# Kernel optimization log

Measured on AMD Instinct MI355X. Metric: run time of the kernel, lower is better.

The kernel has to match this reference:

```python
import jax, jax.numpy as jnp
import numpy as np

THRESHOLD = 0.5
EPS = 1e-6


def setup_inputs() -> dict:
    key = jax.random.key(0)
    k1, k2, k3 = jax.random.split(key, 3)
    B, C, T = 32, 6, 64
    K, N = 8, 128
    S, P = 32, 64
    points = jax.random.normal(k1, (B, C, T, 2), dtype=jnp.float32)
    road_boundary = jax.random.normal(k2, (B, K, N, 2), dtype=jnp.float32)
    centerlines = jax.random.normal(k3, (B, S, P, 2), dtype=jnp.float32)
    return {"points": points, "road_boundary": road_boundary, "centerlines": centerlines}


def _cross(v1, v2):
    return v1[..., 0] * v2[..., 1] - v1[..., 1] * v2[..., 0]


def reference(points, road_boundary, centerlines):
    B, C, T, _ = points.shape
    _, K, N, _ = road_boundary.shape
    _, S, P, _ = centerlines.shape

    # --- min distance to boundary segments ---
    seg_a = road_boundary[:, :, :-1, :]          # (B,K,N-1,2)
    seg_d = road_boundary[:, :, 1:, :] - seg_a   # (B,K,N-1,2)

    p = points[:, None, :, :, None, :]           # (B,1,C,T,1,2)
    a = seg_a[:, :, None, None, :, :]            # (B,K,1,1,N-1,2)
    d = seg_d[:, :, None, None, :, :]            # (B,K,1,1,N-1,2)

    v1 = p - a                                   # (B,K,C,T,N-1,2)
    dot = (v1 * d).sum(-1)                       # (B,K,C,T,N-1)
    edge_sq = (d * d).sum(-1)                    # (B,K,1,1,N-1)
    proj = jnp.clip(dot / (edge_sq + EPS), 0.0, 1.0)
    closest = a + d * proj[..., None]            # (B,K,C,T,N-1,2)
    dist = jnp.sqrt(((p - closest) ** 2).sum(-1))  # (B,K,C,T,N-1)
    min_dist = dist.min(axis=-1).min(axis=1)     # (B,C,T)

    # --- nearest centerline point ---
    cl = centerlines.reshape(B, S * P, 2)        # (B,SP,2)
    v2 = points[:, None, :, :, :] - cl[:, :, None, None, :]  # (B,SP,C,T,2)
    cl_dist_sq = (v2 ** 2).sum(-1)               # (B,SP,C,T)
    idx = jnp.argmin(cl_dist_sq, axis=1)         # (B,C,T)
    closest_cl = cl[jnp.arange(B)[:, None, None], idx]  # (B,C,T,2)

    # --- segment intersection test: (point -> nearest centerline pt) vs boundary edges ---
    a1 = points[:, None, None, :, :, :]          # (B,1,1,C,T,2)
    a2 = closest_cl[:, None, None, :, :, :]      # (B,1,1,C,T,2)
    b1 = seg_a[:, :, :, None, None, :]           # (B,K,N-1,1,1,2)
    db = seg_d[:, :, :, None, None, :]           # (B,K,N-1,1,1,2)

    da = a2 - a1
    dp = a1 - b1                                 # (B,K,N-1,C,T,2)
    dadb = _cross(da, db)                        # (B,K,N-1,C,T)
    t = _cross(da, dp) / (dadb + EPS)
    u = _cross(db, dp) / (dadb + EPS)
    intersect = (t >= 0.0) & (t <= 1.0) & (u >= 0.0) & (u <= 1.0)

    inside = ~jnp.any(intersect, axis=(1, 2))    # (B,C,T)
    min_dist = jnp.where(inside, -min_dist, min_dist)
    return jax.nn.relu(min_dist + THRESHOLD).sum(-1)  # (B,C)
```

## Files before the change

### kernel.cpp

```cpp
#include <hip/hip_runtime.h>

constexpr int cB = 32, cC = 6, cT = 64;
constexpr int cK = 8, cN = 128;
constexpr int cS = 32, cP = 64;
constexpr int NSEG_PAD = cK * cN;
constexpr int NCL  = cS * cP;
constexpr int G = 4;
constexpr int PPW = 4;
constexpr int NIT = NSEG_PAD / 64;
constexpr float F_EPS = 1e-6f;
constexpr float F_THRESHOLD = 0.5f;

__global__ __launch_bounds__(256) void offroad_kernel(
    const float* __restrict__ points,
    const float* __restrict__ road_boundary,
    const float* __restrict__ centerlines,
    float* __restrict__ out)
{
    const int blk  = blockIdx.x;
    const int g    = blk & (G - 1);
    const int bc   = blk >> 2;
    const int b    = bc / cC;
    const int lane = threadIdx.x & 63;
    const int wave = threadIdx.x >> 6;

    const float2* __restrict__ rb2 =
        (const float2*)(road_boundary + (size_t)b * cK * cN * 2);
    const float4* __restrict__ cl4 =
        (const float4*)(centerlines + (size_t)b * NCL * 2);

    const int t0 = (g << 4) | (wave << 2);
    const float* pb = points + (((size_t)bc) * cT + t0) * 2;
    float px[PPW], py[PPW];
    #pragma unroll
    for (int p = 0; p < PPW; ++p) { px[p] = pb[2 * p]; py[p] = pb[2 * p + 1]; }

    float min_d2[PPW], best_d2[PPW];
    int   best_i[PPW];
    #pragma unroll
    for (int p = 0; p < PPW; ++p) {
        min_d2[p] = 3.4e38f; best_d2[p] = 3.4e38f; best_i[p] = 0x7fffffff;
    }

    int s = lane;
    float2 a  = rb2[s];
    float2 nx = rb2[s + (((s & (cN - 1)) < cN - 1) ? 1 : 0)];
    float4 cp = cl4[s];

    #pragma unroll 4
    for (int i = 0; i < NIT; ++i) {
        const float2 ac = a;  const float2 nxc = nx;  const float4 cpc = cp;
        const int    sc = s;
        s += 64;
        if (i < NIT - 1) {
            a  = rb2[s];
            nx = rb2[s + (((s & (cN - 1)) < cN - 1) ? 1 : 0)];
            cp = cl4[s];
        }

        const float dx = nxc.x - ac.x, dy = nxc.y - ac.y;
        const float inv_e2 = __builtin_amdgcn_rcpf(dx * dx + dy * dy + F_EPS);
        const int ia = 2 * sc;

        #pragma unroll
        for (int p = 0; p < PPW; ++p) {
            float v1x = px[p] - ac.x, v1y = py[p] - ac.y;
            float proj = (v1x * dx + v1y * dy) * inv_e2;
            proj = fminf(fmaxf(proj, 0.0f), 1.0f);
            float ex = v1x - dx * proj;
            float ey = v1y - dy * proj;
            min_d2[p] = fminf(min_d2[p], ex * ex + ey * ey);

            float dxa = px[p] - cpc.x, dya = py[p] - cpc.y;
            float d2a = dxa * dxa + dya * dya;
            float dxb = px[p] - cpc.z, dyb = py[p] - cpc.w;
            float d2b = dxb * dxb + dyb * dyb;
            float dmin = d2a; int imin = ia;
            if (d2b < d2a) { dmin = d2b; imin = ia + 1; }
            if (dmin < best_d2[p] ||
                (dmin == best_d2[p] && imin < best_i[p])) {
                best_d2[p] = dmin; best_i[p] = imin;
            }
        }
    }

    #pragma unroll
    for (int off = 1; off <= 32; off <<= 1) {
        #pragma unroll
        for (int p = 0; p < PPW; ++p) {
            float od2 = __shfl_xor(best_d2[p], off);
            int   oi  = __shfl_xor(best_i[p], off);
            if (od2 < best_d2[p] || (od2 == best_d2[p] && oi < best_i[p])) {
                best_d2[p] = od2; best_i[p] = oi;
            }
        }
    }

    const float2* __restrict__ cl2 = (const float2*)cl4;
    float dax[PPW], day[PPW];
    #pragma unroll
    for (int p = 0; p < PPW; ++p) {
        float2 cc = cl2[best_i[p]];
        dax[p] = cc.x - px[p]; day[p] = cc.y - py[p];
    }

    int hit[PPW] = {0, 0, 0, 0};
    s = lane;
    a  = rb2[s];
    nx = rb2[s + (((s & (cN - 1)) < cN - 1) ? 1 : 0)];

    #pragma unroll 4
    for (int i = 0; i < NIT; ++i) {
        const float2 ac = a;  const float2 nxc = nx;
        const int    sc = s;
        s += 64;
        if (i < NIT - 1) {
            a  = rb2[s];
            nx = rb2[s + (((s & (cN - 1)) < cN - 1) ? 1 : 0)];
        }

        const float dbx = nxc.x - ac.x, dby = nxc.y - ac.y;
        const int valid = ((sc & (cN - 1)) < cN - 1) ? 1 : 0;

        #pragma unroll
        for (int p = 0; p < PPW; ++p) {
            float dpx = px[p] - ac.x, dpy = py[p] - ac.y;
            float w  = dax[p] * dby - day[p] * dbx + F_EPS;
            float w2 = w * w;
            float ct = (dax[p] * dpy - day[p] * dpx) * w;
            float cu = (dbx * dpy - dby * dpx) * w;
            bool inb = (ct >= 0.0f) & (ct <= w2) & (cu >= 0.0f) & (cu <= w2);
            hit[p] |= valid & (int)inb;
        }
    }

    #pragma unroll
    for (int off = 1; off <= 32; off <<= 1) {
        #pragma unroll
        for (int p = 0; p < PPW; ++p) {
            min_d2[p] = fminf(min_d2[p], __shfl_xor(min_d2[p], off));
            hit[p]   |= __shfl_xor(hit[p], off);
        }
    }

    float total = 0.0f;
    #pragma unroll
    for (int p = 0; p < PPW; ++p) {
        float md = sqrtf(min_d2[p]);
        float sd = hit[p] ? md : -md;
        total += fmaxf(sd + F_THRESHOLD, 0.0f);
    }
    if (lane == 0)
        atomicAdd(&out[bc], total);
}

extern "C" void kernel_launch(void* const* d_in, const int* in_sizes, int n_in,
                              void* d_out, int out_size, void* d_ws, size_t ws_size,
                              hipStream_t stream) {
    const float* points      = (const float*)d_in[0];
    const float* boundary    = (const float*)d_in[1];
    const float* centerlines = (const float*)d_in[2];
    float* out = (float*)d_out;
    hipMemsetAsync(out, 0, (size_t)out_size * sizeof(float), stream);
    offroad_kernel<<<cB * cC * G, 256, 0, stream>>>(points, boundary, centerlines, out);
}
```

Before: 83.78 us.

## Fuse boundary distance into intersection pass and share segment endpoints via shuffles

Moves the min-distance-to-boundary computation out of the centerline argmin loop and into the intersection loop, so both boundary computations reuse the same segment vectors and v1 differences. Each segment's next endpoint now comes from a wavefront shuffle (shfl_down plus a broadcast of the next chunk's first point) instead of a second global load. The projection clamp uses fmed3. The intersection loop gets heavier per iteration, and shuffle latency is added in exchange for fewer memory loads and redundant arithmetic.

```diff
diff --git a/kernel.cpp b/kernel.cpp
--- a/kernel.cpp
+++ b/kernel.cpp
@@ -35,55 +35,36 @@
     #pragma unroll
     for (int p = 0; p < PPW; ++p) { px[p] = pb[2 * p]; py[p] = pb[2 * p + 1]; }
 
-    float min_d2[PPW], best_d2[PPW];
+    float best_d2[PPW];
     int   best_i[PPW];
     #pragma unroll
-    for (int p = 0; p < PPW; ++p) {
-        min_d2[p] = 3.4e38f; best_d2[p] = 3.4e38f; best_i[p] = 0x7fffffff;
-    }
+    for (int p = 0; p < PPW; ++p) { best_d2[p] = 3.4e38f; best_i[p] = 0x7fffffff; }
 
-    int s = lane;
-    float2 a  = rb2[s];
-    float2 nx = rb2[s + (((s & (cN - 1)) < cN - 1) ? 1 : 0)];
-    float4 cp = cl4[s];
-
-    #pragma unroll 4
-    for (int i = 0; i < NIT; ++i) {
-        const float2 ac = a;  const float2 nxc = nx;  const float4 cpc = cp;
-        const int    sc = s;
-        s += 64;
-        if (i < NIT - 1) {
-            a  = rb2[s];
-            nx = rb2[s + (((s & (cN - 1)) < cN - 1) ? 1 : 0)];
-            cp = cl4[s];
-        }
-
-        const float dx = nxc.x - ac.x, dy = nxc.y - ac.y;
-        const float inv_e2 = __builtin_amdgcn_rcpf(dx * dx + dy * dy + F_EPS);
-        const int ia = 2 * sc;
-
-        #pragma unroll
-        for (int p = 0; p < PPW; ++p) {
-            float v1x = px[p] - ac.x, v1y = py[p] - ac.y;
-            float proj = (v1x * dx + v1y * dy) * inv_e2;
-            proj = fminf(fmaxf(proj, 0.0f), 1.0f);
-            float ex = v1x - dx * proj;
-            float ey = v1y - dy * proj;
-            min_d2[p] = fminf(min_d2[p], ex * ex + ey * ey);
-
-            float dxa = px[p] - cpc.x, dya = py[p] - cpc.y;
-            float d2a = dxa * dxa + dya * dya;
-            float dxb = px[p] - cpc.z, dyb = py[p] - cpc.w;
-            float d2b = dxb * dxb + dyb * dyb;
-            float dmin = d2a; int imin = ia;
-            if (d2b < d2a) { dmin = d2b; imin = ia + 1; }
-            if (dmin < best_d2[p] ||
-                (dmin == best_d2[p] && imin < best_i[p])) {
-                best_d2[p] = dmin; best_i[p] = imin;
+    {
+        int s = lane;
+        float4 cp = cl4[s];
+        #pragma unroll 4
+        for (int i = 0; i < NIT; ++i) {
+            const float4 cpc = cp;
+            const int sc = s;
+            s += 64;
+            if (i < NIT - 1) cp = cl4[s];
+            const int ia = 2 * sc;
+            #pragma unroll
+            for (int p = 0; p < PPW; ++p) {
+                float dxa = px[p] - cpc.x, dya = py[p] - cpc.y;
+                float d2a = dxa * dxa + dya * dya;
+                float dxb = px[p] - cpc.z, dyb = py[p] - cpc.w;
+                float d2b = dxb * dxb + dyb * dyb;
+                float dmin = d2a; int imin = ia;
+                if (d2b < d2a) { dmin = d2b; imin = ia + 1; }
+                if (dmin < best_d2[p] ||
+                    (dmin == best_d2[p] && imin < best_i[p])) {
+                    best_d2[p] = dmin; best_i[p] = imin;
+                }
             }
         }
     }
-
     #pragma unroll
     for (int off = 1; off <= 32; off <<= 1) {
         #pragma unroll
@@ -95,7 +76,6 @@
             }
         }
     }
-
     const float2* __restrict__ cl2 = (const float2*)cl4;
     float dax[PPW], day[PPW];
     #pragma unroll
@@ -104,33 +84,52 @@
         dax[p] = cc.x - px[p]; day[p] = cc.y - py[p];
     }
 
-    int hit[PPW] = {0, 0, 0, 0};
-    s = lane;
-    a  = rb2[s];
-    nx = rb2[s + (((s & (cN - 1)) < cN - 1) ? 1 : 0)];
+    float min_d2[PPW];
+    int   hit[PPW];
+    #pragma unroll
+    for (int p = 0; p < PPW; ++p) { min_d2[p] = 3.4e38f; hit[p] = 0; }
 
-    #pragma unroll 4
-    for (int i = 0; i < NIT; ++i) {
-        const float2 ac = a;  const float2 nxc = nx;
-        const int    sc = s;
-        s += 64;
-        if (i < NIT - 1) {
-            a  = rb2[s];
-            nx = rb2[s + (((s & (cN - 1)) < cN - 1) ? 1 : 0)];
-        }
+    {
+        int s = lane;
+        float2 a = rb2[s];
+        #pragma unroll 2
+        for (int i = 0; i < NIT; ++i) {
+            const float2 ac = a;
+            s += 64;
+            float2 an = ac;
+            if (i < NIT - 1) an = rb2[s];
 
-        const float dbx = nxc.x - ac.x, dby = nxc.y - ac.y;
-        const int valid = ((sc & (cN - 1)) < cN - 1) ? 1 : 0;
+            float sd_x = __shfl_down(ac.x, 1);
+            float sd_y = __shfl_down(ac.y, 1);
+            float b0x  = __shfl(an.x, 0);
+            float b0y  = __shfl(an.y, 0);
+            const bool last = (lane == 63);
+            const bool odd  = (i & 1) != 0;
+            float nx_x = last ? (odd ? ac.x : b0x) : sd_x;
+            float nx_y = last ? (odd ? ac.y : b0y) : sd_y;
+            const int valid = (last && odd) ? 0 : 1;
 
-        #pragma unroll
-        for (int p = 0; p < PPW; ++p) {
-            float dpx = px[p] - ac.x, dpy = py[p] - ac.y;
-            float w  = dax[p] * dby - day[p] * dbx + F_EPS;
-            float w2 = w * w;
-            float ct = (dax[p] * dpy - day[p] * dpx) * w;
-            float cu = (dbx * dpy - dby * dpx) * w;
-            bool inb = (ct >= 0.0f) & (ct <= w2) & (cu >= 0.0f) & (cu <= w2);
-            hit[p] |= valid & (int)inb;
+            a = an;
+
+            const float dx = nx_x - ac.x, dy = nx_y - ac.y;
+            const float inv_e2 =
+                __builtin_amdgcn_rcpf(dx * dx + dy * dy + F_EPS);
+
+            #pragma unroll
+            for (int p = 0; p < PPW; ++p) {
+                float v1x = px[p] - ac.x, v1y = py[p] - ac.y;
+                float proj = (v1x * dx + v1y * dy) * inv_e2;
+                proj = __builtin_amdgcn_fmed3f(proj, 0.0f, 1.0f);
+                float ex = v1x - dx * proj;
+                float ey = v1y - dy * proj;
+                min_d2[p] = fminf(min_d2[p], ex * ex + ey * ey);
+                float w  = dax[p] * dy - day[p] * dx + F_EPS;
+                float w2 = w * w;
+                float ct = (dax[p] * v1y - day[p] * v1x) * w;
+                float cu = (dx * v1y - dy * v1x) * w;
+                bool inb = (ct >= 0.0f) & (ct <= w2) & (cu >= 0.0f) & (cu <= w2);
+                hit[p] |= valid & (int)inb;
+            }
         }
     }
 
```

Measured after the change: 82.17 us. No clear change (-1.9%).
